# Performance work log

Hardware: AMD Instinct MI355X
Metric: run time of the kernel (lower is better)

## Reference

```python
import jax, jax.numpy as jnp
import numpy as np

T, E, DIM, HID = 8192, 8, 1024, 2048


def setup_inputs() -> dict:
    key = jax.random.key(0)
    k1, k2, k3 = jax.random.split(key, 3)
    x = jax.random.normal(k1, (T, DIM), dtype=jnp.float32)
    w1 = jax.random.normal(k2, (E, HID, DIM), dtype=jnp.float32)
    w2 = jax.random.normal(k3, (E, DIM, HID), dtype=jnp.float32)
    # Tokens are pre-grouped by expert; counts must sum exactly to T.
    num_tokens_per_expert = jnp.full((E,), T // E, dtype=jnp.int32)
    return {"x": x, "w1": w1, "w2": w2, "num_tokens_per_expert": num_tokens_per_expert}


def reference(x, w1, w2, num_tokens_per_expert):
    # Faithful to torch._grouped_mm path: bf16 casts, two ragged grouped GEMMs,
    # result cast back to x.dtype.
    gs = num_tokens_per_expert.astype(jnp.int32)
    xb = x.astype(jnp.bfloat16)                                  # [T, dim]
    w1t = jnp.swapaxes(w1.astype(jnp.bfloat16), -2, -1)          # [E, dim, hid]
    w2t = jnp.swapaxes(w2.astype(jnp.bfloat16), -2, -1)          # [E, hid, dim]
    h = jax.lax.ragged_dot(xb, w1t, gs)                          # [T, hid] bf16
    out = jax.lax.ragged_dot(h, w2t, gs)                         # [T, dim] bf16
    return out.astype(x.dtype)
```

## Files before the change

kernel.cpp:

```cpp
#include <hip/hip_runtime.h>
#include <stdint.h>

#define T_TOK 8192
#define NEXP  8
#define DIMSZ 1024
#define HIDSZ 2048

typedef __attribute__((ext_vector_type(4))) float f32x4;
typedef __attribute__((ext_vector_type(8))) short s16x8;


__device__ __forceinline__ uint16_t f2bf(float f) {
  uint32_t u = __builtin_bit_cast(uint32_t, f);
  u += 0x7fffu + ((u >> 16) & 1u);
  return (uint16_t)(u >> 16);
}

__device__ __forceinline__ void gload_lds16(const uint16_t* g, const uint16_t* lds_base) {
  __builtin_amdgcn_global_load_lds(
      (const __attribute__((address_space(1))) uint32_t*)(uintptr_t)g,
      (__attribute__((address_space(3))) uint32_t*)(uint32_t)(uintptr_t)lds_base,
      16, 0, 0);
}


__global__ void cvt_f32_to_bf16(const float* __restrict__ in,
                                uint16_t* __restrict__ out, int n8) {
  int stride = gridDim.x * blockDim.x;
  for (int i = blockIdx.x * blockDim.x + threadIdx.x; i < n8; i += stride) {
    const float4* p = (const float4*)in + 2 * (size_t)i;
    float4 a = p[0], b = p[1];
    uint4 o;
    o.x = f2bf(a.x) | ((uint32_t)f2bf(a.y) << 16);
    o.y = f2bf(a.z) | ((uint32_t)f2bf(a.w) << 16);
    o.z = f2bf(b.x) | ((uint32_t)f2bf(b.y) << 16);
    o.w = f2bf(b.z) | ((uint32_t)f2bf(b.w) << 16);
    ((uint4*)out)[i] = o;
  }
}

__global__ void offs_kernel(const int* __restrict__ counts, int* __restrict__ offs) {
  if (threadIdx.x == 0 && blockIdx.x == 0) {
    int s = 0;
    for (int e = 0; e < NEXP; ++e) { offs[e] = s; s += counts[e]; }
    offs[NEXP] = s;
  }
}

template <bool OUT_BF16>
__global__ void gemm_grouped(const uint16_t* __restrict__ A,
                             const uint16_t* __restrict__ B,
                             void* __restrict__ C,
                             const int* __restrict__ offs,
                             int N, int K) {
  __shared__ __align__(16) uint16_t As[128 * 32];
  __shared__ __align__(16) uint16_t Bs[128 * 32];

  const int maxMT = T_TOK / 128;
  const int e  = blockIdx.y / maxMT;
  const int mt = blockIdx.y % maxMT;
  const int m_start = offs[e];
  const int m_count = offs[e + 1] - m_start;
  const int m0 = mt * 128;
  if (m0 >= m_count) return;
  int valid_m = m_count - m0;
  if (valid_m > 128) valid_m = 128;
  const int n0 = blockIdx.x * 128;

  const int tid  = threadIdx.x;
  const int w    = tid >> 6;
  const int lane = tid & 63;
  const int wm = w & 1, wn = w >> 1;

  const int srow0 = w * 16 + (lane >> 2);
  const int srow1 = (w + 4) * 16 + (lane >> 2);
  const int scol  = (lane & 3) * 8;

  const uint16_t* gA = A + (size_t)m_start * K;
  const uint16_t* gB = B + (size_t)e * N * K;

  const int ar0 = m0 + (srow0 < valid_m ? srow0 : valid_m - 1);
  const int ar1 = m0 + (srow1 < valid_m ? srow1 : valid_m - 1);

  const uint16_t* a0p = gA + (size_t)ar0 * K + scol;
  const uint16_t* a1p = gA + (size_t)ar1 * K + scol;
  const uint16_t* b0p = gB + (size_t)(n0 + srow0) * K + scol;
  const uint16_t* b1p = gB + (size_t)(n0 + srow1) * K + scol;

  const uint16_t* lA0 = &As[w * 512];
  const uint16_t* lA1 = &As[(w + 4) * 512];
  const uint16_t* lB0 = &Bs[w * 512];
  const uint16_t* lB1 = &Bs[(w + 4) * 512];

  const int fr = lane & 15;
  const int fk = (lane >> 4) * 8;

  f32x4 acc[4][4];
#pragma unroll
  for (int mi = 0; mi < 4; ++mi)
#pragma unroll
    for (int ni = 0; ni < 4; ++ni) acc[mi][ni] = (f32x4){0.f, 0.f, 0.f, 0.f};

  for (int k0 = 0; k0 < K; k0 += 32) {
    __syncthreads();
    gload_lds16(a0p, lA0);
    gload_lds16(a1p, lA1);
    gload_lds16(b0p, lB0);
    gload_lds16(b1p, lB1);
    a0p += 32; a1p += 32; b0p += 32; b1p += 32;
    __syncthreads();

    s16x8 af[4], bf[4];
#pragma unroll
    for (int mi = 0; mi < 4; ++mi)
      af[mi] = *(const s16x8*)&As[(wm * 64 + mi * 16 + fr) * 32 + fk];
#pragma unroll
    for (int ni = 0; ni < 4; ++ni)
      bf[ni] = *(const s16x8*)&Bs[(wn * 64 + ni * 16 + fr) * 32 + fk];
#pragma unroll
    for (int mi = 0; mi < 4; ++mi)
#pragma unroll
      for (int ni = 0; ni < 4; ++ni)
        acc[mi][ni] = __builtin_amdgcn_mfma_f32_16x16x32_bf16(af[mi], bf[ni], acc[mi][ni], 0, 0, 0);
  }

  const int cq = (lane >> 4) * 4;
  const int cc = lane & 15;
#pragma unroll
  for (int mi = 0; mi < 4; ++mi) {
#pragma unroll
    for (int r = 0; r < 4; ++r) {
      const int rt = wm * 64 + mi * 16 + cq + r;
      if (rt < valid_m) {
        const size_t rowoff = (size_t)(m_start + m0 + rt) * N;
#pragma unroll
        for (int ni = 0; ni < 4; ++ni) {
          const int col = n0 + wn * 64 + ni * 16 + cc;
          const float v = acc[mi][ni][r];
          if (OUT_BF16) {
            ((uint16_t*)C)[rowoff + col] = f2bf(v);
          } else {
            const uint32_t b = (uint32_t)f2bf(v) << 16;
            ((float*)C)[rowoff + col] = __builtin_bit_cast(float, b);
          }
        }
      }
    }
  }
}


extern "C" void kernel_launch(void* const* d_in, const int* in_sizes, int n_in,
                              void* d_out, int out_size, void* d_ws, size_t ws_size,
                              hipStream_t stream) {
  const float* x  = (const float*)d_in[0];
  const float* w1 = (const float*)d_in[1];
  const float* w2 = (const float*)d_in[2];
  const int* cnt  = (const int*)d_in[3];
  float* out = (float*)d_out;

  char* ws = (char*)d_ws;
  uint16_t* xb  = (uint16_t*)(ws);
  uint16_t* w1b = (uint16_t*)(ws + 16777216);
  uint16_t* w2b = (uint16_t*)(ws + 50331648);
  uint16_t* h   = (uint16_t*)(ws + 83886080);
  int* offs     = (int*)(ws + 117440512);

  offs_kernel<<<1, 64, 0, stream>>>(cnt, offs);
  cvt_f32_to_bf16<<<1024, 256, 0, stream>>>(x,  xb,  (T_TOK * DIMSZ) / 8);
  cvt_f32_to_bf16<<<2048, 256, 0, stream>>>(w1, w1b, (NEXP * HIDSZ * DIMSZ) / 8);
  cvt_f32_to_bf16<<<2048, 256, 0, stream>>>(w2, w2b, (NEXP * DIMSZ * HIDSZ) / 8);

  dim3 g1(HIDSZ / 128, NEXP * (T_TOK / 128));
  gemm_grouped<true><<<g1, 256, 0, stream>>>(xb, w1b, (void*)h, offs, HIDSZ, DIMSZ);

  dim3 g2(DIMSZ / 128, NEXP * (T_TOK / 128));
  gemm_grouped<false><<<g2, 256, 0, stream>>>(h, w2b, (void*)out, offs, DIMSZ, HIDSZ);
}
```

Before: 317.0 us.

## Compact grouped GEMM grid, swizzle LDS layout, fuse conversion kernels

Folds the offset computation and the three fp32-to-bf16 conversions into one kernel, which also builds per-expert tile offsets. Each grouped GEMM now runs on a compact 1D grid, so only real M tiles are launched instead of the full expert×64 tile grid with early exits. N tiles become the fast-varying index, so neighbouring blocks share A rows. An XOR swizzle on the LDS column index is meant to cut bank conflicts on the fragment reads, and launch_bounds is set to 4 blocks per CU.

```diff
diff --git a/kernel.cpp b/kernel.cpp
--- a/kernel.cpp
+++ b/kernel.cpp
@@ -24,48 +24,60 @@
 }
 
 
-__global__ void cvt_f32_to_bf16(const float* __restrict__ in,
-                                uint16_t* __restrict__ out, int n8) {
-  int stride = gridDim.x * blockDim.x;
-  for (int i = blockIdx.x * blockDim.x + threadIdx.x; i < n8; i += stride) {
-    const float4* p = (const float4*)in + 2 * (size_t)i;
+__global__ void cvt_all(const float* __restrict__ x, const float* __restrict__ w1,
+                        const float* __restrict__ w2, uint16_t* __restrict__ xb,
+                        uint16_t* __restrict__ w1b, uint16_t* __restrict__ w2b,
+                        const int* __restrict__ counts, int* __restrict__ offs,
+                        int* __restrict__ toffs) {
+  if (blockIdx.x == 0 && threadIdx.x == 0) {
+    int s = 0, ts = 0;
+    for (int e = 0; e < NEXP; ++e) {
+      offs[e] = s; toffs[e] = ts;
+      s += counts[e]; ts += (counts[e] + 127) >> 7;
+    }
+    offs[NEXP] = s; toffs[NEXP] = ts;
+  }
+  const int NX = (T_TOK * DIMSZ) / 8;
+  const int NW = (NEXP * HIDSZ * DIMSZ) / 8;
+  const int total = NX + 2 * NW;
+  const int stride = gridDim.x * blockDim.x;
+  for (int i = blockIdx.x * blockDim.x + threadIdx.x; i < total; i += stride) {
+    const float* src; uint16_t* dst; int j;
+    if (i < NX)           { src = x;  dst = xb;  j = i; }
+    else if (i < NX + NW) { src = w1; dst = w1b; j = i - NX; }
+    else                  { src = w2; dst = w2b; j = i - NX - NW; }
+    const float4* p = (const float4*)src + 2 * (size_t)j;
     float4 a = p[0], b = p[1];
     uint4 o;
     o.x = f2bf(a.x) | ((uint32_t)f2bf(a.y) << 16);
     o.y = f2bf(a.z) | ((uint32_t)f2bf(a.w) << 16);
     o.z = f2bf(b.x) | ((uint32_t)f2bf(b.y) << 16);
     o.w = f2bf(b.z) | ((uint32_t)f2bf(b.w) << 16);
-    ((uint4*)out)[i] = o;
-  }
-}
-
-__global__ void offs_kernel(const int* __restrict__ counts, int* __restrict__ offs) {
-  if (threadIdx.x == 0 && blockIdx.x == 0) {
-    int s = 0;
-    for (int e = 0; e < NEXP; ++e) { offs[e] = s; s += counts[e]; }
-    offs[NEXP] = s;
+    ((uint4*)dst)[j] = o;
   }
 }
 
 template <bool OUT_BF16>
-__global__ void gemm_grouped(const uint16_t* __restrict__ A,
-                             const uint16_t* __restrict__ B,
-                             void* __restrict__ C,
-                             const int* __restrict__ offs,
-                             int N, int K) {
+__global__ __launch_bounds__(256, 4)
+void gemm_grouped(const uint16_t* __restrict__ A, const uint16_t* __restrict__ B,
+                  void* __restrict__ C, const int* __restrict__ offs,
+                  const int* __restrict__ toffs, int N, int K, int lognt) {
   __shared__ __align__(16) uint16_t As[128 * 32];
   __shared__ __align__(16) uint16_t Bs[128 * 32];
 
-  const int maxMT = T_TOK / 128;
-  const int e  = blockIdx.y / maxMT;
-  const int mt = blockIdx.y % maxMT;
+  const int mtg = blockIdx.x >> lognt;
+  const int nt  = blockIdx.x & ((1 << lognt) - 1);
+  if (mtg >= toffs[NEXP]) return;
+  int e = 0;
+#pragma unroll
+  for (int i = 1; i < NEXP; ++i) e += (toffs[i] <= mtg) ? 1 : 0;
+  const int mt      = mtg - toffs[e];
   const int m_start = offs[e];
   const int m_count = offs[e + 1] - m_start;
-  const int m0 = mt * 128;
-  if (m0 >= m_count) return;
+  const int m0      = mt * 128;
   int valid_m = m_count - m0;
   if (valid_m > 128) valid_m = 128;
-  const int n0 = blockIdx.x * 128;
+  const int n0 = nt * 128;
 
   const int tid  = threadIdx.x;
   const int w    = tid >> 6;
@@ -74,7 +86,7 @@
 
   const int srow0 = w * 16 + (lane >> 2);
   const int srow1 = (w + 4) * 16 + (lane >> 2);
-  const int scol  = (lane & 3) * 8;
+  const int scol  = (((lane & 3) ^ ((lane >> 3) & 3))) * 8;
 
   const uint16_t* gA = A + (size_t)m_start * K;
   const uint16_t* gB = B + (size_t)e * N * K;
@@ -92,8 +104,8 @@
   const uint16_t* lB0 = &Bs[w * 512];
   const uint16_t* lB1 = &Bs[(w + 4) * 512];
 
-  const int fr = lane & 15;
-  const int fk = (lane >> 4) * 8;
+  const int fr  = lane & 15;
+  const int fk  = ((lane >> 4) ^ ((fr >> 1) & 3)) * 8;
 
   f32x4 acc[4][4];
 #pragma unroll
@@ -165,15 +177,15 @@
   uint16_t* w2b = (uint16_t*)(ws + 50331648);
   uint16_t* h   = (uint16_t*)(ws + 83886080);
   int* offs     = (int*)(ws + 117440512);
+  int* toffs    = offs + 9;
 
-  offs_kernel<<<1, 64, 0, stream>>>(cnt, offs);
-  cvt_f32_to_bf16<<<1024, 256, 0, stream>>>(x,  xb,  (T_TOK * DIMSZ) / 8);
-  cvt_f32_to_bf16<<<2048, 256, 0, stream>>>(w1, w1b, (NEXP * HIDSZ * DIMSZ) / 8);
-  cvt_f32_to_bf16<<<2048, 256, 0, stream>>>(w2, w2b, (NEXP * DIMSZ * HIDSZ) / 8);
+  cvt_all<<<4096, 256, 0, stream>>>(x, w1, w2, xb, w1b, w2b, cnt, offs, toffs);
 
-  dim3 g1(HIDSZ / 128, NEXP * (T_TOK / 128));
-  gemm_grouped<true><<<g1, 256, 0, stream>>>(xb, w1b, (void*)h, offs, HIDSZ, DIMSZ);
+  const int MAX_MT = T_TOK / 128 + NEXP - 1;
 
-  dim3 g2(DIMSZ / 128, NEXP * (T_TOK / 128));
-  gemm_grouped<false><<<g2, 256, 0, stream>>>(h, w2b, (void*)out, offs, DIMSZ, HIDSZ);
+  gemm_grouped<true><<<MAX_MT * 16, 256, 0, stream>>>(
+      xb, w1b, (void*)h, offs, toffs, HIDSZ, DIMSZ, 4);
+
+  gemm_grouped<false><<<MAX_MT * 8, 256, 0, stream>>>(
+      h, w2b, (void*)out, offs, toffs, DIMSZ, HIDSZ, 3);
 }
```

Measured after the change: 289.7 us. 1.09x faster.
